# Kernel tuning notes

Hardware: AMD Instinct MI355X
Metric: run time of the kernel (lower is better)

## Reference

```python
import jax, jax.numpy as jnp
import numpy as np

DIM_X, DIM_Y, BATCH = 64, 64, 2


def setup_inputs() -> dict:
    key = jax.random.key(0)
    k1, k2, k3 = jax.random.split(key, 3)
    mean_in = jax.random.normal(k1, (BATCH, DIM_X, DIM_Y), dtype=jnp.float32)
    # std must be positive
    std_in = jax.random.uniform(k2, (BATCH, DIM_X, DIM_Y), dtype=jnp.float32, minval=0.1, maxval=1.0)
    # identity correlation matrix -> PSD covariance, valid sqrt/div downstream
    n = DIM_X * DIM_Y
    corr_in = jnp.broadcast_to(jnp.eye(n, dtype=jnp.float32), (BATCH, n, n))
    # kaiming_uniform_(a=sqrt(5)) on a (dx, dy) weight -> bound = 1/sqrt(dy)
    bound = 1.0 / np.sqrt(DIM_Y)
    weight = jax.random.uniform(k3, (DIM_X, DIM_Y), dtype=jnp.float32, minval=-bound, maxval=bound)
    return {"mean_in": mean_in, "std_in": std_in, "corr_in": corr_in, "weight": weight}


def reference(mean_in, std_in, corr_in, weight):
    B, dx, dy = mean_in.shape
    n = dx * dy
    # fft(fft(w, dim=0), dim=1) == 2D FFT
    wfft = jnp.fft.fft2(weight)  # (dx, dy) complex

    # covariance from std and corr: cov[b,i,j,k,l] = std[b,i,j] * corr[b,i,j,k,l] * std[b,k,l]
    corr = corr_in.reshape(B, dx, dy, dx, dy)
    cov = std_in[:, None, None, :, :] * corr * std_in[:, :, :, None, None]

    # mean path: circular 2D convolution via FFT
    mean_fft = jnp.fft.fft2(mean_in, axes=(1, 2))
    mean_out = jnp.real(jnp.fft.ifft2(wfft[None] * mean_fft, axes=(1, 2)))

    # covariance path: 4D FFT, broadcast multiply by wfft on both index pairs, 4D IFFT
    cov_f = jnp.fft.fftn(cov, axes=(1, 2, 3, 4))
    cov_f = wfft[None, None, None, :, :] * cov_f * wfft[None, :, :, None, None]
    cov_out = jnp.real(jnp.fft.ifftn(cov_f, axes=(1, 2, 3, 4)))
    cov_out = cov_out.reshape(B, n, n)

    # update_correlation: std = sqrt(diag(cov)); corr = cov / (std outer std)
    var = jnp.diagonal(cov_out, axis1=-2, axis2=-1)  # (B, n)
    std_out = jnp.sqrt(jnp.maximum(var, 1e-12))
    denom = std_out[:, :, None] * std_out[:, None, :]
    corr_out = cov_out / denom
    std_out = std_out.reshape(B, dx, dy)
    return mean_out, std_out, corr_out
```

## Files before the change

kernel.cpp:

```cpp
#include <hip/hip_runtime.h>
#include <math.h>

#define DXY   64
#define NN    4096
#define NB    2
#define PITCH 65

__device__ __forceinline__ int lpos(int p) {
    return (p >> 6) * PITCH + (p & 63);
}

__device__ void fft64_fwd(float* re, float* im, const float* twr, const float* twi,
                          int es, int rs)
{
#pragma unroll
    for (int s = 0; s < 3; ++s) {
        int len   = 64 >> (2 * s);
        int qsh   = 4 - 2 * s;
        int q     = 1 << qsh;
        int tstep = 1 << (2 * s);
        __syncthreads();
#pragma unroll
        for (int g = threadIdx.x; g < 1024; g += 256) {
            int w = g & 63;
            int f = g >> 6;
            int o = f & (q - 1);
            int base = (f >> qsh) * len;
            int A0 = w * rs + (base + o) * es;
            int A1 = A0 + q * es;
            int A2 = A1 + q * es;
            int A3 = A2 + q * es;
            float a0r = re[A0], a0i = im[A0];
            float a1r = re[A1], a1i = im[A1];
            float a2r = re[A2], a2i = im[A2];
            float a3r = re[A3], a3i = im[A3];
            float t0r = a0r + a2r, t0i = a0i + a2i;
            float t1r = a0r - a2r, t1i = a0i - a2i;
            float t2r = a1r + a3r, t2i = a1i + a3i;
            float dr  = a1r - a3r, di  = a1i - a3i;
            float t3r = di,        t3i = -dr;
            float b0r = t0r + t2r, b0i = t0i + t2i;
            float b1r = t1r + t3r, b1i = t1i + t3i;
            float b2r = t0r - t2r, b2i = t0i - t2i;
            float b3r = t1r - t3r, b3i = t1i - t3i;
            int k1 = o * tstep, k2 = k1 + k1, k3 = k2 + k1;
            float c1 = twr[k1], s1 = twi[k1];
            float c2 = twr[k2], s2 = twi[k2];
            float c3 = twr[k3], s3 = twi[k3];
            re[A0] = b0r;                 im[A0] = b0i;
            re[A1] = b1r * c1 - b1i * s1; im[A1] = b1r * s1 + b1i * c1;
            re[A2] = b2r * c2 - b2i * s2; im[A2] = b2r * s2 + b2i * c2;
            re[A3] = b3r * c3 - b3i * s3; im[A3] = b3r * s3 + b3i * c3;
        }
    }
}

__device__ void fft64_inv(float* re, float* im, const float* twr, const float* twi,
                          int es, int rs)
{
#pragma unroll
    for (int s = 0; s < 3; ++s) {
        int len   = 4 << (2 * s);
        int qsh   = 2 * s;
        int q     = 1 << qsh;
        int tstep = 16 >> (2 * s);
        __syncthreads();
#pragma unroll
        for (int g = threadIdx.x; g < 1024; g += 256) {
            int w = g & 63;
            int f = g >> 6;
            int o = f & (q - 1);
            int base = (f >> qsh) * len;
            int A0 = w * rs + (base + o) * es;
            int A1 = A0 + q * es;
            int A2 = A1 + q * es;
            int A3 = A2 + q * es;
            int k1 = o * tstep, k2 = k1 + k1, k3 = k2 + k1;
            float c1 = twr[k1], s1 = -twi[k1];
            float c2 = twr[k2], s2 = -twi[k2];
            float c3 = twr[k3], s3 = -twi[k3];
            float a0r = re[A0], a0i = im[A0];
            float x1r = re[A1], x1i = im[A1];
            float x2r = re[A2], x2i = im[A2];
            float x3r = re[A3], x3i = im[A3];
            float a1r = x1r * c1 - x1i * s1, a1i = x1r * s1 + x1i * c1;
            float a2r = x2r * c2 - x2i * s2, a2i = x2r * s2 + x2i * c2;
            float a3r = x3r * c3 - x3i * s3, a3i = x3r * s3 + x3i * c3;
            float t0r = a0r + a2r, t0i = a0i + a2i;
            float t1r = a0r - a2r, t1i = a0i - a2i;
            float t2r = a1r + a3r, t2i = a1i + a3i;
            float dr  = a1r - a3r, di  = a1i - a3i;
            float t3r = -di,       t3i = dr;
            re[A0] = t0r + t2r; im[A0] = t0i + t2i;
            re[A1] = t1r + t3r; im[A1] = t1i + t3i;
            re[A2] = t0r - t2r; im[A2] = t0i - t2i;
            re[A3] = t1r - t3r; im[A3] = t1i - t3i;
        }
    }
}

__global__ __launch_bounds__(256)
void row_conv2_kernel(const float* __restrict__ in, float* __restrict__ out,
                      const float2* __restrict__ wfft_br,
                      const float* __restrict__ sstd,
                      float* var_out)
{
    __shared__ float re[DXY * PITCH];
    __shared__ float im[DXY * PITCH];
    __shared__ float twr[64], twi[64];

    int tid  = threadIdx.x;
    int row0 = 2 * blockIdx.x;
    long long off0 = (long long)row0 * NN;
    long long off1 = off0 + NN;
    int b   = row0 >> 12;
    int rI0 = row0 & (NN - 1);
    int rI1 = rI0 + 1;

    if (tid < 64) {
        float ang = -6.28318530717958647692f * (float)tid / 64.0f;
        twr[tid] = cosf(ang);
        twi[tid] = sinf(ang);
    }

    float sI0 = 1.0f, sI1 = 1.0f;
    const float* sb = nullptr;
    if (sstd) {
        sb  = sstd + (long long)b * NN;
        sI0 = sb[rI0];
        sI1 = sb[rI1];
    }

#pragma unroll
    for (int i = 0; i < 4; ++i) {
        int p = (tid + 256 * i) * 4;
        float4 a = *(const float4*)(in + off0 + p);
        float4 c = *(const float4*)(in + off1 + p);
        if (sb) {
            float4 s4 = *(const float4*)(sb + p);
            a.x *= sI0 * s4.x; a.y *= sI0 * s4.y; a.z *= sI0 * s4.z; a.w *= sI0 * s4.w;
            c.x *= sI1 * s4.x; c.y *= sI1 * s4.y; c.z *= sI1 * s4.z; c.w *= sI1 * s4.w;
        }
        int q0 = lpos(p);
        re[q0] = a.x; re[q0+1] = a.y; re[q0+2] = a.z; re[q0+3] = a.w;
        im[q0] = c.x; im[q0+1] = c.y; im[q0+2] = c.z; im[q0+3] = c.w;
    }

    fft64_fwd(re, im, twr, twi, 1, PITCH);
    fft64_fwd(re, im, twr, twi, PITCH, 1);
    __syncthreads();

#pragma unroll
    for (int i = 0; i < 16; ++i) {
        int p = tid + 256 * i;
        float2 wv = wfft_br[p];
        int a = lpos(p);
        float xr = re[a], xi = im[a];
        re[a] = xr * wv.x - xi * wv.y;
        im[a] = xr * wv.y + xi * wv.x;
    }

    fft64_inv(re, im, twr, twi, PITCH, 1);
    fft64_inv(re, im, twr, twi, 1, PITCH);
    __syncthreads();

    const float scale = 1.0f / 4096.0f;
#pragma unroll
    for (int i = 0; i < 4; ++i) {
        int p = (tid + 256 * i) * 4;
        int q0 = lpos(p);
        float4 a, c;
        a.x = re[q0] * scale; a.y = re[q0+1] * scale;
        a.z = re[q0+2] * scale; a.w = re[q0+3] * scale;
        c.x = im[q0] * scale; c.y = im[q0+1] * scale;
        c.z = im[q0+2] * scale; c.w = im[q0+3] * scale;
        *(float4*)(out + off0 + p) = a;
        *(float4*)(out + off1 + p) = c;
    }
    if (var_out && tid == 0) {
        var_out[row0]     = re[lpos(rI0)] * scale;
        var_out[row0 + 1] = im[lpos(rI1)] * scale;
    }
}

__global__ __launch_bounds__(256)
void wfft_kernel(const float* __restrict__ w, float2* wfft_br)
{
    __shared__ float re[DXY * PITCH];
    __shared__ float im[DXY * PITCH];
    __shared__ float twr[64], twi[64];
    int tid = threadIdx.x;
    if (tid < 64) {
        float ang = -6.28318530717958647692f * (float)tid / 64.0f;
        twr[tid] = cosf(ang);
        twi[tid] = sinf(ang);
    }
#pragma unroll
    for (int i = 0; i < 16; ++i) {
        int p = tid + 256 * i;
        re[lpos(p)] = w[p];
        im[lpos(p)] = 0.0f;
    }
    fft64_fwd(re, im, twr, twi, 1, PITCH);
    fft64_fwd(re, im, twr, twi, PITCH, 1);
    __syncthreads();
#pragma unroll
    for (int i = 0; i < 16; ++i) {
        int p = tid + 256 * i;
        wfft_br[p] = make_float2(re[lpos(p)], im[lpos(p)]);
    }
}

__global__ __launch_bounds__(256)
void transpose_inplace_kernel(float* data)
{
    int bx = blockIdx.x, by = blockIdx.y, b = blockIdx.z;
    if (by > bx) return;
    __shared__ float tA[64][PITCH];
    __shared__ float tB[64][PITCH];
    int tx = threadIdx.x & 63, ty = threadIdx.x >> 6;
    long long base = (long long)b * NN * NN;
    float* A  = data + base + (long long)(by * 64) * NN + bx * 64;
    float* Bt = data + base + (long long)(bx * 64) * NN + by * 64;
    if (bx == by) {
        for (int r = ty; r < 64; r += 4) tA[r][tx] = A[(long long)r * NN + tx];
        __syncthreads();
        for (int r = ty; r < 64; r += 4) A[(long long)r * NN + tx] = tA[tx][r];
    } else {
        for (int r = ty; r < 64; r += 4) {
            tA[r][tx] = A[(long long)r * NN + tx];
            tB[r][tx] = Bt[(long long)r * NN + tx];
        }
        __syncthreads();
        for (int r = ty; r < 64; r += 4) {
            A[(long long)r * NN + tx]  = tB[tx][r];
            Bt[(long long)r * NN + tx] = tA[tx][r];
        }
    }
}

__global__ __launch_bounds__(256)
void norm_transpose_inplace_kernel(float* data, const float* __restrict__ rstd)
{
    int bx = blockIdx.x, by = blockIdx.y, b = blockIdx.z;
    if (by > bx) return;
    __shared__ float tA[64][PITCH];
    __shared__ float tB[64][PITCH];
    int tx = threadIdx.x & 63, ty = threadIdx.x >> 6;
    long long base = (long long)b * NN * NN;
    const float* rs = rstd + (long long)b * NN;
    float* A  = data + base + (long long)(by * 64) * NN + bx * 64;
    float* Bt = data + base + (long long)(bx * 64) * NN + by * 64;
    float rcA = rs[bx * 64 + tx];
    float rcB = rs[by * 64 + tx];
    if (bx == by) {
        for (int r = ty; r < 64; r += 4) tA[r][tx] = A[(long long)r * NN + tx];
        __syncthreads();
        for (int r = ty; r < 64; r += 4)
            A[(long long)r * NN + tx] = tA[tx][r] * rs[by * 64 + r] * rcA;
    } else {
        for (int r = ty; r < 64; r += 4) {
            tA[r][tx] = A[(long long)r * NN + tx];
            tB[r][tx] = Bt[(long long)r * NN + tx];
        }
        __syncthreads();
        for (int r = ty; r < 64; r += 4) {
            A[(long long)r * NN + tx]  = tB[tx][r] * rs[by * 64 + r] * rcA;
            Bt[(long long)r * NN + tx] = tA[tx][r] * rs[bx * 64 + r] * rcB;
        }
    }
}

__global__ __launch_bounds__(256)
void std_kernel(const float* __restrict__ var, float* std_out, float* rstd, int n)
{
    int i = blockIdx.x * 256 + threadIdx.x;
    if (i < n) {
        float s = sqrtf(fmaxf(var[i], 1e-12f));
        std_out[i] = s;
        rstd[i] = 1.0f / s;
    }
}

extern "C" void kernel_launch(void* const* d_in, const int* in_sizes, int n_in,
                              void* d_out, int out_size, void* d_ws, size_t ws_size,
                              hipStream_t stream)
{
    const float* mean_in = (const float*)d_in[0];
    const float* std_in  = (const float*)d_in[1];
    const float* corr_in = (const float*)d_in[2];
    const float* weight  = (const float*)d_in[3];

    float* out      = (float*)d_out;
    float* mean_out = out;
    float* std_out  = out + 8192;
    float* corr_out = out + 16384;

    float*  ws      = (float*)d_ws;
    float2* wfft_br = (float2*)ws;
    float*  var_ws  = ws + 8192;
    float*  rstd_ws = ws + 16384;

    wfft_kernel<<<1, 256, 0, stream>>>(weight, wfft_br);

    row_conv2_kernel<<<1, 256, 0, stream>>>(mean_in, mean_out, wfft_br,
                                            nullptr, nullptr);

    row_conv2_kernel<<<NB * NN / 2, 256, 0, stream>>>(corr_in, corr_out, wfft_br,
                                                      std_in, nullptr);

    dim3 tg(64, 64, NB);
    transpose_inplace_kernel<<<tg, 256, 0, stream>>>(corr_out);

    row_conv2_kernel<<<NB * NN / 2, 256, 0, stream>>>(corr_out, corr_out, wfft_br,
                                                      nullptr, var_ws);

    std_kernel<<<(NB * NN + 255) / 256, 256, 0, stream>>>(var_ws, std_out,
                                                          rstd_ws, NB * NN);

    norm_transpose_inplace_kernel<<<tg, 256, 0, stream>>>(corr_out, rstd_ws);
}
```

Before: 509.7 us.

## Rewrite 64x64 FFT as register radix-16x4 passes and vectorize transposes

The shared-memory radix-4 FFT stages, each separated by a barrier, are replaced by a 4x16 decomposition. Each thread holds 16 complex values in registers, runs a hard-coded radix-16 kernel, and exchanges data through one interleaved float2 shared buffer. The frequency-domain weight multiply is folded into the second forward pass, and launch bounds now request four blocks per CU. The in-place transpose and normalize-transpose kernels switch to float4 global loads and stores with transposed shared writes. This aims to cut barriers, twiddle table reads and global memory transactions, at the cost of higher register pressure and possible LDS bank conflicts from the strided float2 accesses.

```diff
diff --git a/kernel.cpp b/kernel.cpp
--- a/kernel.cpp
+++ b/kernel.cpp
@@ -4,210 +4,225 @@
 #define DXY   64
 #define NN    4096
 #define NB    2
-#define PITCH 65
-
-__device__ __forceinline__ int lpos(int p) {
-    return (p >> 6) * PITCH + (p & 63);
-}
-
-__device__ void fft64_fwd(float* re, float* im, const float* twr, const float* twi,
-                          int es, int rs)
-{
-#pragma unroll
-    for (int s = 0; s < 3; ++s) {
-        int len   = 64 >> (2 * s);
-        int qsh   = 4 - 2 * s;
-        int q     = 1 << qsh;
-        int tstep = 1 << (2 * s);
-        __syncthreads();
-#pragma unroll
-        for (int g = threadIdx.x; g < 1024; g += 256) {
-            int w = g & 63;
-            int f = g >> 6;
-            int o = f & (q - 1);
-            int base = (f >> qsh) * len;
-            int A0 = w * rs + (base + o) * es;
-            int A1 = A0 + q * es;
-            int A2 = A1 + q * es;
-            int A3 = A2 + q * es;
-            float a0r = re[A0], a0i = im[A0];
-            float a1r = re[A1], a1i = im[A1];
-            float a2r = re[A2], a2i = im[A2];
-            float a3r = re[A3], a3i = im[A3];
-            float t0r = a0r + a2r, t0i = a0i + a2i;
-            float t1r = a0r - a2r, t1i = a0i - a2i;
-            float t2r = a1r + a3r, t2i = a1i + a3i;
-            float dr  = a1r - a3r, di  = a1i - a3i;
-            float t3r = di,        t3i = -dr;
-            float b0r = t0r + t2r, b0i = t0i + t2i;
-            float b1r = t1r + t3r, b1i = t1i + t3i;
-            float b2r = t0r - t2r, b2i = t0i - t2i;
-            float b3r = t1r - t3r, b3i = t1i - t3i;
-            int k1 = o * tstep, k2 = k1 + k1, k3 = k2 + k1;
-            float c1 = twr[k1], s1 = twi[k1];
-            float c2 = twr[k2], s2 = twi[k2];
-            float c3 = twr[k3], s3 = twi[k3];
-            re[A0] = b0r;                 im[A0] = b0i;
-            re[A1] = b1r * c1 - b1i * s1; im[A1] = b1r * s1 + b1i * c1;
-            re[A2] = b2r * c2 - b2i * s2; im[A2] = b2r * s2 + b2i * c2;
-            re[A3] = b3r * c3 - b3i * s3; im[A3] = b3r * s3 + b3i * c3;
-        }
-    }
-}
-
-__device__ void fft64_inv(float* re, float* im, const float* twr, const float* twi,
-                          int es, int rs)
-{
-#pragma unroll
-    for (int s = 0; s < 3; ++s) {
-        int len   = 4 << (2 * s);
-        int qsh   = 2 * s;
-        int q     = 1 << qsh;
-        int tstep = 16 >> (2 * s);
-        __syncthreads();
-#pragma unroll
-        for (int g = threadIdx.x; g < 1024; g += 256) {
-            int w = g & 63;
-            int f = g >> 6;
-            int o = f & (q - 1);
-            int base = (f >> qsh) * len;
-            int A0 = w * rs + (base + o) * es;
-            int A1 = A0 + q * es;
-            int A2 = A1 + q * es;
-            int A3 = A2 + q * es;
-            int k1 = o * tstep, k2 = k1 + k1, k3 = k2 + k1;
-            float c1 = twr[k1], s1 = -twi[k1];
-            float c2 = twr[k2], s2 = -twi[k2];
-            float c3 = twr[k3], s3 = -twi[k3];
-            float a0r = re[A0], a0i = im[A0];
-            float x1r = re[A1], x1i = im[A1];
-            float x2r = re[A2], x2i = im[A2];
-            float x3r = re[A3], x3i = im[A3];
-            float a1r = x1r * c1 - x1i * s1, a1i = x1r * s1 + x1i * c1;
-            float a2r = x2r * c2 - x2i * s2, a2i = x2r * s2 + x2i * c2;
-            float a3r = x3r * c3 - x3i * s3, a3i = x3r * s3 + x3i * c3;
-            float t0r = a0r + a2r, t0i = a0i + a2i;
-            float t1r = a0r - a2r, t1i = a0i - a2i;
-            float t2r = a1r + a3r, t2i = a1i + a3i;
-            float dr  = a1r - a3r, di  = a1i - a3i;
-            float t3r = -di,       t3i = dr;
-            re[A0] = t0r + t2r; im[A0] = t0i + t2i;
-            re[A1] = t1r + t3r; im[A1] = t1i + t3i;
-            re[A2] = t0r - t2r; im[A2] = t0i - t2i;
-            re[A3] = t1r - t3r; im[A3] = t1i - t3i;
-        }
-    }
-}
-
-__global__ __launch_bounds__(256)
+#define CP    65
+
+#define C16 0.9238795325112867f
+#define S16 0.3826834323650898f
+#define R22 0.7071067811865476f
+
+__device__ __forceinline__ void cmul_ip(float2& a, float wr, float wi) {
+    float t = a.x * wr - a.y * wi;
+    a.y = a.x * wi + a.y * wr;
+    a.x = t;
+}
+
+__device__ __forceinline__ void bf4(float2* y, int i0, int i1, int i2, int i3, int inv) {
+    float2 a0 = y[i0], a1 = y[i1], a2 = y[i2], a3 = y[i3];
+    float t0r = a0.x + a2.x, t0i = a0.y + a2.y;
+    float t1r = a0.x - a2.x, t1i = a0.y - a2.y;
+    float t2r = a1.x + a3.x, t2i = a1.y + a3.y;
+    float dr  = a1.x - a3.x, di  = a1.y - a3.y;
+    float t3r, t3i;
+    if (inv) { t3r = -di; t3i = dr; } else { t3r = di; t3i = -dr; }
+    y[i0] = make_float2(t0r + t2r, t0i + t2i);
+    y[i1] = make_float2(t1r + t3r, t1i + t3i);
+    y[i2] = make_float2(t0r - t2r, t0i - t2i);
+    y[i3] = make_float2(t1r - t3r, t1i - t3i);
+}
+
+__device__ __forceinline__ void fft16_fwd(float2* y) {
+    bf4(y, 0, 4, 8, 12, 0);
+    bf4(y, 1, 5, 9, 13, 0);
+    cmul_ip(y[5],  C16, -S16); cmul_ip(y[9],  R22, -R22); cmul_ip(y[13],  S16, -C16);
+    bf4(y, 2, 6, 10, 14, 0);
+    cmul_ip(y[6],  R22, -R22); cmul_ip(y[10], 0.f, -1.f); cmul_ip(y[14], -R22, -R22);
+    bf4(y, 3, 7, 11, 15, 0);
+    cmul_ip(y[7],  S16, -C16); cmul_ip(y[11], -R22, -R22); cmul_ip(y[15], -C16,  S16);
+    bf4(y, 0, 1, 2, 3, 0); bf4(y, 4, 5, 6, 7, 0);
+    bf4(y, 8, 9, 10, 11, 0); bf4(y, 12, 13, 14, 15, 0);
+}
+
+__device__ __forceinline__ void fft16_inv(float2* y) {
+    bf4(y, 0, 1, 2, 3, 1); bf4(y, 4, 5, 6, 7, 1);
+    bf4(y, 8, 9, 10, 11, 1); bf4(y, 12, 13, 14, 15, 1);
+    cmul_ip(y[5],  C16,  S16); cmul_ip(y[9],  R22,  R22); cmul_ip(y[13],  S16,  C16);
+    cmul_ip(y[6],  R22,  R22); cmul_ip(y[10], 0.f,  1.f); cmul_ip(y[14], -R22,  R22);
+    cmul_ip(y[7],  S16,  C16); cmul_ip(y[11], -R22,  R22); cmul_ip(y[15], -C16, -S16);
+    bf4(y, 0, 4, 8, 12, 1); bf4(y, 1, 5, 9, 13, 1);
+    bf4(y, 2, 6, 10, 14, 1); bf4(y, 3, 7, 11, 15, 1);
+}
+
+template<int US, int NS, bool FUSEW>
+__device__ void fwd_pass(float2* z, const float2* __restrict__ wf, int u, int k1,
+                         float c1r, float c1i, float s2, float2 Wb)
+{
+    const int B = u * US;
+    float2 y[16];
+    float twr = 1.f, twi = 0.f;
+#pragma unroll
+    for (int n2 = 0; n2 < 16; ++n2) {
+        float2 x0 = z[B + n2 * NS];
+        float2 x1 = z[B + (n2 + 16) * NS];
+        float2 x2 = z[B + (n2 + 32) * NS];
+        float2 x3 = z[B + (n2 + 48) * NS];
+        float er  = fmaf(s2, x2.x, x0.x), ei = fmaf(s2, x2.y, x0.y);
+        float orr = fmaf(s2, x3.x, x1.x), oi = fmaf(s2, x3.y, x1.y);
+        float br = er + c1r * orr - c1i * oi;
+        float bi = ei + c1r * oi + c1i * orr;
+        y[n2].x = twr * br - twi * bi;
+        y[n2].y = twr * bi + twi * br;
+        float t = twr * Wb.x - twi * Wb.y;
+        twi = twr * Wb.y + twi * Wb.x;
+        twr = t;
+    }
+    fft16_fwd(y);
+    if (FUSEW) {
+#pragma unroll
+        for (int p = 0; p < 16; ++p) {
+            float2 wv = wf[(16 * k1 + p) * 64 + u];
+            cmul_ip(y[p], wv.x, wv.y);
+        }
+    }
+    __syncthreads();
+#pragma unroll
+    for (int p = 0; p < 16; ++p) z[B + (16 * k1 + p) * NS] = y[p];
+    __syncthreads();
+}
+
+template<int US, int NS>
+__device__ void inv_pass(float2* z, int u, int k1,
+                         float ci1r, float ci1i, float s2, float2 Wbc)
+{
+    const int B = u * US;
+    float2 y[16];
+#pragma unroll
+    for (int p = 0; p < 16; ++p) y[p] = z[B + (16 * k1 + p) * NS];
+    fft16_inv(y);
+    float twr = 1.f, twi = 0.f;
+#pragma unroll
+    for (int n2 = 0; n2 < 16; ++n2) {
+        cmul_ip(y[n2], twr, twi);
+        float t = twr * Wbc.x - twi * Wbc.y;
+        twi = twr * Wbc.y + twi * Wbc.x;
+        twr = t;
+    }
+#pragma unroll
+    for (int n2 = 0; n2 < 16; ++n2) z[B + (16 * k1 + n2) * NS] = y[n2];
+    __syncthreads();
+    float2 xx[16];
+#pragma unroll
+    for (int n2 = 0; n2 < 16; ++n2) {
+        float2 h0 = z[B + n2 * NS];
+        float2 h1 = z[B + (n2 + 16) * NS];
+        float2 h2 = z[B + (n2 + 32) * NS];
+        float2 h3 = z[B + (n2 + 48) * NS];
+        float er  = fmaf(s2, h2.x, h0.x), ei = fmaf(s2, h2.y, h0.y);
+        float orr = fmaf(s2, h3.x, h1.x), oi = fmaf(s2, h3.y, h1.y);
+        xx[n2].x = er + ci1r * orr - ci1i * oi;
+        xx[n2].y = ei + ci1r * oi + ci1i * orr;
+    }
+    __syncthreads();
+#pragma unroll
+    for (int n2 = 0; n2 < 16; ++n2) z[B + (16 * k1 + n2) * NS] = xx[n2];
+    __syncthreads();
+}
+
+__global__ __launch_bounds__(256, 4)
 void row_conv2_kernel(const float* __restrict__ in, float* __restrict__ out,
                       const float2* __restrict__ wfft_br,
-                      const float* __restrict__ sstd,
-                      float* var_out)
-{
-    __shared__ float re[DXY * PITCH];
-    __shared__ float im[DXY * PITCH];
-    __shared__ float twr[64], twi[64];
-
-    int tid  = threadIdx.x;
-    int row0 = 2 * blockIdx.x;
-    long long off0 = (long long)row0 * NN;
-    long long off1 = off0 + NN;
-    int b   = row0 >> 12;
-    int rI0 = row0 & (NN - 1);
-    int rI1 = rI0 + 1;
-
-    if (tid < 64) {
-        float ang = -6.28318530717958647692f * (float)tid / 64.0f;
-        twr[tid] = cosf(ang);
-        twi[tid] = sinf(ang);
-    }
-
-    float sI0 = 1.0f, sI1 = 1.0f;
+                      const float* __restrict__ sstd, float* var_out)
+{
+    __shared__ float2 z[64 * CP];
+    const int tid = threadIdx.x;
+    const int u   = ((tid >> 6) << 4) | (tid & 15);
+    const int k1  = (tid >> 4) & 3;
+    const float c1r = (k1 == 0) ? 1.f : ((k1 == 2) ? -1.f : 0.f);
+    const float c1i = (k1 == 1) ? -1.f : ((k1 == 3) ? 1.f : 0.f);
+    const float s2  = (k1 & 1) ? -1.f : 1.f;
+    const float ang = -0.09817477042468103f * (float)k1;
+    const float2 Wb  = make_float2(cosf(ang), sinf(ang));
+    const float2 Wbc = make_float2(Wb.x, -Wb.y);
+    const float ci1r = c1r, ci1i = -c1i;
+
+    const int row0 = 2 * blockIdx.x;
+    const long long off0 = (long long)row0 * NN, off1 = off0 + NN;
+    const int b   = row0 >> 12;
+    const int rI0 = row0 & (NN - 1), rI1 = rI0 + 1;
     const float* sb = nullptr;
-    if (sstd) {
-        sb  = sstd + (long long)b * NN;
-        sI0 = sb[rI0];
-        sI1 = sb[rI1];
-    }
+    float sI0 = 1.f, sI1 = 1.f;
+    if (sstd) { sb = sstd + (long long)b * NN; sI0 = sb[rI0]; sI1 = sb[rI1]; }
 
 #pragma unroll
     for (int i = 0; i < 4; ++i) {
-        int p = (tid + 256 * i) * 4;
-        float4 a = *(const float4*)(in + off0 + p);
-        float4 c = *(const float4*)(in + off1 + p);
+        int idx = tid + 256 * i;
+        int p = idx * 4;
+        int r = p >> 6, c = p & 63;
+        float4 a  = *(const float4*)(in + off0 + p);
+        float4 cc = *(const float4*)(in + off1 + p);
         if (sb) {
             float4 s4 = *(const float4*)(sb + p);
             a.x *= sI0 * s4.x; a.y *= sI0 * s4.y; a.z *= sI0 * s4.z; a.w *= sI0 * s4.w;
-            c.x *= sI1 * s4.x; c.y *= sI1 * s4.y; c.z *= sI1 * s4.z; c.w *= sI1 * s4.w;
-        }
-        int q0 = lpos(p);
-        re[q0] = a.x; re[q0+1] = a.y; re[q0+2] = a.z; re[q0+3] = a.w;
-        im[q0] = c.x; im[q0+1] = c.y; im[q0+2] = c.z; im[q0+3] = c.w;
-    }
-
-    fft64_fwd(re, im, twr, twi, 1, PITCH);
-    fft64_fwd(re, im, twr, twi, PITCH, 1);
-    __syncthreads();
+            cc.x *= sI1 * s4.x; cc.y *= sI1 * s4.y; cc.z *= sI1 * s4.z; cc.w *= sI1 * s4.w;
+        }
+        float2* zp = z + r * CP + c;
+        zp[0] = make_float2(a.x, cc.x);
+        zp[1] = make_float2(a.y, cc.y);
+        zp[2] = make_float2(a.z, cc.z);
+        zp[3] = make_float2(a.w, cc.w);
+    }
+    __syncthreads();
+
+    fwd_pass<CP, 1, false>(z, nullptr,  u, k1, c1r, c1i, s2, Wb);
+    fwd_pass<1, CP, true >(z, wfft_br,  u, k1, c1r, c1i, s2, Wb);
+    inv_pass<1, CP>(z, u, k1, ci1r, ci1i, s2, Wbc);
+    inv_pass<CP, 1>(z, u, k1, ci1r, ci1i, s2, Wbc);
+
+    const float scale = 1.0f / 4096.0f;
+#pragma unroll
+    for (int i = 0; i < 4; ++i) {
+        int idx = tid + 256 * i;
+        int p = idx * 4;
+        int r = p >> 6, c = p & 63;
+        const float2* zp = z + r * CP + c;
+        float4 a, cc;
+        a.x = zp[0].x * scale; a.y = zp[1].x * scale;
+        a.z = zp[2].x * scale; a.w = zp[3].x * scale;
+        cc.x = zp[0].y * scale; cc.y = zp[1].y * scale;
+        cc.z = zp[2].y * scale; cc.w = zp[3].y * scale;
+        *(float4*)(out + off0 + p) = a;
+        *(float4*)(out + off1 + p) = cc;
+    }
+    if (var_out && tid == 0) {
+        var_out[row0]     = z[(rI0 >> 6) * CP + (rI0 & 63)].x * scale;
+        var_out[row0 + 1] = z[(rI1 >> 6) * CP + (rI1 & 63)].y * scale;
+    }
+}
+
+__global__ __launch_bounds__(256, 4)
+void wfft_kernel(const float* __restrict__ w, float2* wfft_br)
+{
+    __shared__ float2 z[64 * CP];
+    const int tid = threadIdx.x;
+    const int u   = ((tid >> 6) << 4) | (tid & 15);
+    const int k1  = (tid >> 4) & 3;
+    const float c1r = (k1 == 0) ? 1.f : ((k1 == 2) ? -1.f : 0.f);
+    const float c1i = (k1 == 1) ? -1.f : ((k1 == 3) ? 1.f : 0.f);
+    const float s2  = (k1 & 1) ? -1.f : 1.f;
+    const float ang = -0.09817477042468103f * (float)k1;
+    const float2 Wb = make_float2(cosf(ang), sinf(ang));
 
 #pragma unroll
     for (int i = 0; i < 16; ++i) {
         int p = tid + 256 * i;
-        float2 wv = wfft_br[p];
-        int a = lpos(p);
-        float xr = re[a], xi = im[a];
-        re[a] = xr * wv.x - xi * wv.y;
-        im[a] = xr * wv.y + xi * wv.x;
-    }
-
-    fft64_inv(re, im, twr, twi, PITCH, 1);
-    fft64_inv(re, im, twr, twi, 1, PITCH);
-    __syncthreads();
-
-    const float scale = 1.0f / 4096.0f;
-#pragma unroll
-    for (int i = 0; i < 4; ++i) {
-        int p = (tid + 256 * i) * 4;
-        int q0 = lpos(p);
-        float4 a, c;
-        a.x = re[q0] * scale; a.y = re[q0+1] * scale;
-        a.z = re[q0+2] * scale; a.w = re[q0+3] * scale;
-        c.x = im[q0] * scale; c.y = im[q0+1] * scale;
-        c.z = im[q0+2] * scale; c.w = im[q0+3] * scale;
-        *(float4*)(out + off0 + p) = a;
-        *(float4*)(out + off1 + p) = c;
-    }
-    if (var_out && tid == 0) {
-        var_out[row0]     = re[lpos(rI0)] * scale;
-        var_out[row0 + 1] = im[lpos(rI1)] * scale;
-    }
-}
-
-__global__ __launch_bounds__(256)
-void wfft_kernel(const float* __restrict__ w, float2* wfft_br)
-{
-    __shared__ float re[DXY * PITCH];
-    __shared__ float im[DXY * PITCH];
-    __shared__ float twr[64], twi[64];
-    int tid = threadIdx.x;
-    if (tid < 64) {
-        float ang = -6.28318530717958647692f * (float)tid / 64.0f;
-        twr[tid] = cosf(ang);
-        twi[tid] = sinf(ang);
-    }
+        z[(p >> 6) * CP + (p & 63)] = make_float2(w[p], 0.f);
+    }
+    __syncthreads();
+    fwd_pass<CP, 1, false>(z, nullptr, u, k1, c1r, c1i, s2, Wb);
+    fwd_pass<1, CP, false>(z, nullptr, u, k1, c1r, c1i, s2, Wb);
 #pragma unroll
     for (int i = 0; i < 16; ++i) {
         int p = tid + 256 * i;
-        re[lpos(p)] = w[p];
-        im[lpos(p)] = 0.0f;
-    }
-    fft64_fwd(re, im, twr, twi, 1, PITCH);
-    fft64_fwd(re, im, twr, twi, PITCH, 1);
-    __syncthreads();
-#pragma unroll
-    for (int i = 0; i < 16; ++i) {
-        int p = tid + 256 * i;
-        wfft_br[p] = make_float2(re[lpos(p)], im[lpos(p)]);
+        wfft_br[p] = z[(p >> 6) * CP + (p & 63)];
     }
 }
 
@@ -216,25 +231,52 @@
 {
     int bx = blockIdx.x, by = blockIdx.y, b = blockIdx.z;
     if (by > bx) return;
-    __shared__ float tA[64][PITCH];
-    __shared__ float tB[64][PITCH];
-    int tx = threadIdx.x & 63, ty = threadIdx.x >> 6;
+    __shared__ float tA[64 * 65];
+    __shared__ float tB[64 * 65];
+    const int f  = threadIdx.x & 15;
+    const int r0 = threadIdx.x >> 4;
     long long base = (long long)b * NN * NN;
     float* A  = data + base + (long long)(by * 64) * NN + bx * 64;
     float* Bt = data + base + (long long)(bx * 64) * NN + by * 64;
     if (bx == by) {
-        for (int r = ty; r < 64; r += 4) tA[r][tx] = A[(long long)r * NN + tx];
+#pragma unroll
+        for (int it = 0; it < 4; ++it) {
+            int r = r0 + 16 * it;
+            float4 v = *(const float4*)(A + (long long)r * NN + 4 * f);
+            tA[(4 * f + 0) * 65 + r] = v.x; tA[(4 * f + 1) * 65 + r] = v.y;
+            tA[(4 * f + 2) * 65 + r] = v.z; tA[(4 * f + 3) * 65 + r] = v.w;
+        }
         __syncthreads();
-        for (int r = ty; r < 64; r += 4) A[(long long)r * NN + tx] = tA[tx][r];
+#pragma unroll
+        for (int it = 0; it < 4; ++it) {
+            int c = r0 + 16 * it;
+            float4 v;
+            v.x = tA[c * 65 + 4 * f + 0]; v.y = tA[c * 65 + 4 * f + 1];
+            v.z = tA[c * 65 + 4 * f + 2]; v.w = tA[c * 65 + 4 * f + 3];
+            *(float4*)(A + (long long)c * NN + 4 * f) = v;
+        }
     } else {
-        for (int r = ty; r < 64; r += 4) {
-            tA[r][tx] = A[(long long)r * NN + tx];
-            tB[r][tx] = Bt[(long long)r * NN + tx];
+#pragma unroll
+        for (int it = 0; it < 4; ++it) {
+            int r = r0 + 16 * it;
+            float4 v = *(const float4*)(A + (long long)r * NN + 4 * f);
+            float4 w = *(const float4*)(Bt + (long long)r * NN + 4 * f);
+            tA[(4 * f + 0) * 65 + r] = v.x; tA[(4 * f + 1) * 65 + r] = v.y;
+            tA[(4 * f + 2) * 65 + r] = v.z; tA[(4 * f + 3) * 65 + r] = v.w;
+            tB[(4 * f + 0) * 65 + r] = w.x; tB[(4 * f + 1) * 65 + r] = w.y;
+            tB[(4 * f + 2) * 65 + r] = w.z; tB[(4 * f + 3) * 65 + r] = w.w;
         }
         __syncthreads();
-        for (int r = ty; r < 64; r += 4) {
-            A[(long long)r * NN + tx]  = tB[tx][r];
-            Bt[(long long)r * NN + tx] = tA[tx][r];
+#pragma unroll
+        for (int it = 0; it < 4; ++it) {
+            int c = r0 + 16 * it;
+            float4 v, w;
+            v.x = tB[c * 65 + 4 * f + 0]; v.y = tB[c * 65 + 4 * f + 1];
+            v.z = tB[c * 65 + 4 * f + 2]; v.w = tB[c * 65 + 4 * f + 3];
+            w.x = tA[c * 65 + 4 * f + 0]; w.y = tA[c * 65 + 4 * f + 1];
+            w.z = tA[c * 65 + 4 * f + 2]; w.w = tA[c * 65 + 4 * f + 3];
+            *(float4*)(A + (long long)c * NN + 4 * f)  = v;
+            *(float4*)(Bt + (long long)c * NN + 4 * f) = w;
         }
     }
 }
@@ -244,29 +286,64 @@
 {
     int bx = blockIdx.x, by = blockIdx.y, b = blockIdx.z;
     if (by > bx) return;
-    __shared__ float tA[64][PITCH];
-    __shared__ float tB[64][PITCH];
-    int tx = threadIdx.x & 63, ty = threadIdx.x >> 6;
+    __shared__ float tA[64 * 65];
+    __shared__ float tB[64 * 65];
+    const int f  = threadIdx.x & 15;
+    const int r0 = threadIdx.x >> 4;
     long long base = (long long)b * NN * NN;
     const float* rs = rstd + (long long)b * NN;
     float* A  = data + base + (long long)(by * 64) * NN + bx * 64;
     float* Bt = data + base + (long long)(bx * 64) * NN + by * 64;
-    float rcA = rs[bx * 64 + tx];
-    float rcB = rs[by * 64 + tx];
+    float4 rsx_bx = *(const float4*)(rs + bx * 64 + 4 * f);
+    float4 rsx_by = *(const float4*)(rs + by * 64 + 4 * f);
     if (bx == by) {
-        for (int r = ty; r < 64; r += 4) tA[r][tx] = A[(long long)r * NN + tx];
+#pragma unroll
+        for (int it = 0; it < 4; ++it) {
+            int r = r0 + 16 * it;
+            float4 v = *(const float4*)(A + (long long)r * NN + 4 * f);
+            tA[(4 * f + 0) * 65 + r] = v.x; tA[(4 * f + 1) * 65 + r] = v.y;
+            tA[(4 * f + 2) * 65 + r] = v.z; tA[(4 * f + 3) * 65 + r] = v.w;
+        }
         __syncthreads();
-        for (int r = ty; r < 64; r += 4)
-            A[(long long)r * NN + tx] = tA[tx][r] * rs[by * 64 + r] * rcA;
+#pragma unroll
+        for (int it = 0; it < 4; ++it) {
+            int c = r0 + 16 * it;
+            float rr = rs[by * 64 + c];
+            float4 v;
+            v.x = tA[c * 65 + 4 * f + 0] * rr * rsx_bx.x;
+            v.y = tA[c * 65 + 4 * f + 1] * rr * rsx_bx.y;
+            v.z = tA[c * 65 + 4 * f + 2] * rr * rsx_bx.z;
+            v.w = tA[c * 65 + 4 * f + 3] * rr * rsx_bx.w;
+            *(float4*)(A + (long long)c * NN + 4 * f) = v;
+        }
     } else {
-        for (int r = ty; r < 64; r += 4) {
-            tA[r][tx] = A[(long long)r * NN + tx];
-            tB[r][tx] = Bt[(long long)r * NN + tx];
+#pragma unroll
+        for (int it = 0; it < 4; ++it) {
+            int r = r0 + 16 * it;
+            float4 v = *(const float4*)(A + (long long)r * NN + 4 * f);
+            float4 w = *(const float4*)(Bt + (long long)r * NN + 4 * f);
+            tA[(4 * f + 0) * 65 + r] = v.x; tA[(4 * f + 1) * 65 + r] = v.y;
+            tA[(4 * f + 2) * 65 + r] = v.z; tA[(4 * f + 3) * 65 + r] = v.w;
+            tB[(4 * f + 0) * 65 + r] = w.x; tB[(4 * f + 1) * 65 + r] = w.y;
+            tB[(4 * f + 2) * 65 + r] = w.z; tB[(4 * f + 3) * 65 + r] = w.w;
         }
         __syncthreads();
-        for (int r = ty; r < 64; r += 4) {
-            A[(long long)r * NN + tx]  = tB[tx][r] * rs[by * 64 + r] * rcA;
-            Bt[(long long)r * NN + tx] = tA[tx][r] * rs[bx * 64 + r] * rcB;
+#pragma unroll
+        for (int it = 0; it < 4; ++it) {
+            int c = r0 + 16 * it;
+            float rA = rs[by * 64 + c];
+            float rB = rs[bx * 64 + c];
+            float4 v, w;
+            v.x = tB[c * 65 + 4 * f + 0] * rA * rsx_bx.x;
+            v.y = tB[c * 65 + 4 * f + 1] * rA * rsx_bx.y;
+            v.z = tB[c * 65 + 4 * f + 2] * rA * rsx_bx.z;
+            v.w = tB[c * 65 + 4 * f + 3] * rA * rsx_bx.w;
+            w.x = tA[c * 65 + 4 * f + 0] * rB * rsx_by.x;
+            w.y = tA[c * 65 + 4 * f + 1] * rB * rsx_by.y;
+            w.z = tA[c * 65 + 4 * f + 2] * rB * rsx_by.z;
+            w.w = tA[c * 65 + 4 * f + 3] * rB * rsx_by.w;
+            *(float4*)(A + (long long)c * NN + 4 * f)  = v;
+            *(float4*)(Bt + (long long)c * NN + 4 * f) = w;
         }
     }
 }
```

Result: faster. 482.2 us (-5.4%).
